# Kernel optimization log

Measured on AMD Instinct MI355X. Metric: run time of the kernel, lower is better.

## Reference

```python
import jax, jax.numpy as jnp
import numpy as np

MAX_TAG = 16          # tag ids live in [0, MAX_TAG]; 0 = background
NUM_SEG = MAX_TAG + 1
LGG_VALUE = 3.0


def setup_inputs() -> dict:
    key = jax.random.key(0)
    k1, k2, k3 = jax.random.split(key, 3)
    B, C, H, W = 16, 8, 512, 512
    gt_kernel_key = jax.random.randint(k1, (B, H, W), 0, MAX_TAG + 1, dtype=jnp.int32)
    training_mask = jax.random.randint(k2, (B, H, W), 0, 2, dtype=jnp.int32)
    similarity_vector = jax.random.normal(k3, (B, C, H, W), dtype=jnp.float32)
    return {
        "gt_kernel_key": gt_kernel_key,
        "training_mask": training_mask,
        "similarity_vector": similarity_vector,
    }


def _per_sample_loss(sim_hwc, gk, mask):
    # sim_hwc: [H, W, C]; gk, mask: [H, W]
    C = sim_hwc.shape[-1]
    flat_sim = sim_hwc.reshape(-1, C)            # [HW, C]
    flat_gk = gk.reshape(-1)                     # [HW]
    ones = jnp.ones_like(flat_gk, dtype=jnp.float32)

    # segment mean per tag over the UNMASKED kernel map (matches original:
    # tags are selected with the mask, but means use gt_kernel directly)
    sums = jax.ops.segment_sum(flat_sim, flat_gk, num_segments=NUM_SEG)      # [T, C]
    counts = jax.ops.segment_sum(ones, flat_gk, num_segments=NUM_SEG)       # [T]
    means = sums / jnp.maximum(counts, 1.0)[:, None]

    # a tag participates iff it appears in gt_kernel_key * training_mask and != 0
    masked_gk = flat_gk * mask.reshape(-1)
    masked_counts = jax.ops.segment_sum(ones, masked_gk, num_segments=NUM_SEG)
    present = (masked_counts > 0).at[0].set(False)                           # [T]

    # pairwise distances between tag means (tiny: NUM_SEG x NUM_SEG)
    diff = means[:, None, :] - means[None, :, :]                             # [T, T, C]
    dist = jnp.sqrt(jnp.sum(diff * diff, axis=-1) + 1e-12)                   # [T, T]
    pair_loss = jnp.log(jnp.maximum(LGG_VALUE - dist, 0.0) ** 2 + 1.0)

    valid = present[:, None] & present[None, :] & ~jnp.eye(NUM_SEG, dtype=bool)
    n_valid = jnp.sum(valid.astype(jnp.float32))
    loss = jnp.sum(jnp.where(valid, pair_loss, 0.0)) / jnp.maximum(n_valid, 1.0)
    sample_valid = (jnp.sum(present.astype(jnp.int32)) >= 2).astype(jnp.float32)
    return loss, sample_valid


def reference(gt_kernel_key, training_mask, similarity_vector):
    # [B, C, H, W] -> [B, H, W, C]
    sim = jnp.transpose(similarity_vector, (0, 2, 3, 1))
    losses, valids = jax.vmap(_per_sample_loss)(sim, gt_kernel_key, training_mask)
    n = jnp.sum(valids)
    return jnp.where(n > 0, jnp.sum(losses * valids) / jnp.maximum(n, 1.0), 0.0)
```

## Files before the change

### kernel.cpp

```cpp
#include <hip/hip_runtime.h>

#define NB 16
#define NC 8
#define HW (512*512)
#define NT 16
#define LGG 3.0f

#define BLOCKS 2048
#define THREADS 256
#define BPSAMP (BLOCKS/NB)
#define PXB (HW/BPSAMP)
#define PXW (PXB/4)
#define NMFMA (PXW/32)
#define NCOL 10
#define ACCW (NT*NCOL)

typedef __attribute__((ext_vector_type(8))) short bf16x8;
typedef __attribute__((ext_vector_type(4))) float f32x4;

__device__ __forceinline__ unsigned pk_bf16(float x, float y) {
    unsigned r;
    asm("v_cvt_pk_bf16_f32 %0, %1, %2" : "=v"(r) : "v"(x), "v"(y));
    return r;
}

struct Frag { int4 g0, g1, m0, m1; float4 v0, v1; };

__device__ __forceinline__ Frag ldm(const int* gkp, const int* mkp,
                                    const float* sp, int off, int c) {
    Frag f;
    f.g0 = *(const int4*)(gkp + off);
    f.g1 = *(const int4*)(gkp + off + 4);
    if (c < 8) {
        f.v0 = *(const float4*)(sp + off);
        f.v1 = *(const float4*)(sp + off + 4);
    }
    if (c == 9) {
        f.m0 = *(const int4*)(mkp + off);
        f.m1 = *(const int4*)(mkp + off + 4);
    }
    return f;
}

__device__ __forceinline__ unsigned onehot2(int a, int b, int r1) {
    return (a == r1 ? 0x3F80u : 0u) | (b == r1 ? 0x3F800000u : 0u);
}
__device__ __forceinline__ unsigned mask2(int a, int b) {
    return (a ? 0x3F80u : 0u) | (b ? 0x3F800000u : 0u);
}

__device__ __forceinline__ f32x4 step(const Frag& f, int c, int r1, f32x4 acc) {
    union { bf16x8 v; unsigned u[4]; } A, B;
    A.u[0] = onehot2(f.g0.x, f.g0.y, r1);
    A.u[1] = onehot2(f.g0.z, f.g0.w, r1);
    A.u[2] = onehot2(f.g1.x, f.g1.y, r1);
    A.u[3] = onehot2(f.g1.z, f.g1.w, r1);
    const unsigned bs0 = pk_bf16(f.v0.x, f.v0.y), bs1 = pk_bf16(f.v0.z, f.v0.w);
    const unsigned bs2 = pk_bf16(f.v1.x, f.v1.y), bs3 = pk_bf16(f.v1.z, f.v1.w);
    const unsigned bm0 = mask2(f.m0.x, f.m0.y), bm1 = mask2(f.m0.z, f.m0.w);
    const unsigned bm2 = mask2(f.m1.x, f.m1.y), bm3 = mask2(f.m1.z, f.m1.w);
    B.u[0] = c < 8 ? bs0 : (c == 8 ? 0x3F803F80u : (c == 9 ? bm0 : 0u));
    B.u[1] = c < 8 ? bs1 : (c == 8 ? 0x3F803F80u : (c == 9 ? bm1 : 0u));
    B.u[2] = c < 8 ? bs2 : (c == 8 ? 0x3F803F80u : (c == 9 ? bm2 : 0u));
    B.u[3] = c < 8 ? bs3 : (c == 8 ? 0x3F803F80u : (c == 9 ? bm3 : 0u));
    return __builtin_amdgcn_mfma_f32_16x16x32_bf16(A.v, B.v, acc, 0, 0, 0);
}

__global__ __launch_bounds__(256) void init_ws(float* g_acc) {
    const int i = threadIdx.x;
    #pragma unroll
    for (int k = 0; k < NB*ACCW; k += 256)
        if (k + i < NB*ACCW) g_acc[k + i] = 0.f;
}

__global__ __launch_bounds__(THREADS) void accum(
    const int* __restrict__ gk, const int* __restrict__ mask,
    const float* __restrict__ sim, float* __restrict__ g_acc)
{
    const int tid  = threadIdx.x;
    const int lane = tid & 63, wid = tid >> 6;
    const int bid  = blockIdx.x;
    const int b    = bid / BPSAMP;
    const int sb   = bid % BPSAMP;
    const int c    = lane & 15;
    const int l4   = lane >> 4;
    const int p0   = sb * PXB + wid * PXW + l4 * 8;

    const int*   gkp = gk   + (size_t)b * HW + p0;
    const int*   mkp = mask + (size_t)b * HW + p0;
    const float* sp  = sim  + ((size_t)b * NC + (c & 7)) * HW + p0;

    __shared__ float lred[4][256];

    f32x4 acc = {0.f, 0.f, 0.f, 0.f};
    const int r1 = c + 1;

    Frag cur = ldm(gkp, mkp, sp, 0, c);
    #pragma unroll
    for (int it = 0; it < NMFMA; ++it) {
        Frag nxt;
        if (it + 1 < NMFMA) nxt = ldm(gkp, mkp, sp, (it + 1) * 32, c);
        acc = step(cur, c, r1, acc);
        cur = nxt;
    }

    const int row0 = (lane >> 4) * 4;
    #pragma unroll
    for (int i = 0; i < 4; ++i) lred[wid][(row0 + i) * 16 + c] = acc[i];
    __syncthreads();

    if (tid < NT * NCOL) {
        const int r = tid / NCOL, cc = tid % NCOL;
        const float s = lred[0][r*16+cc] + lred[1][r*16+cc]
                      + lred[2][r*16+cc] + lred[3][r*16+cc];
        atomicAdd(&g_acc[b * ACCW + tid], s);
    }
}

__global__ __launch_bounds__(256) void finalize(
    const float* __restrict__ g_acc, float* __restrict__ out)
{
    __shared__ float    means[NB][NT][NC];
    __shared__ unsigned pres[NB];
    __shared__ float    sl[NB], sn[NB];
    const int tid = threadIdx.x;

    if (tid < NB) pres[tid] = 0u;
    __syncthreads();

    {
        const int b = tid >> 4, t = tid & 15;
        const float* row = g_acc + b * ACCW + t * NCOL;
        const float cnt = row[8];
        const float mc  = row[9];
        const float inv = 1.f / fmaxf(cnt, 1.f);
        #pragma unroll
        for (int cc = 0; cc < NC; ++cc) means[b][t][cc] = row[cc] * inv;
        if (mc > 0.5f) atomicOr(&pres[b], 1u << (t + 1));
    }
    __syncthreads();

    const int b = tid >> 4, i = tid & 15;
    const unsigned pr = pres[b];
    float loss = 0.f, nv = 0.f;
    if ((pr >> (i + 1)) & 1u) {
        #pragma unroll
        for (int j = 0; j < NT; ++j) {
            if (j != i && ((pr >> (j + 1)) & 1u)) {
                float d2 = 0.f;
                #pragma unroll
                for (int cc = 0; cc < NC; ++cc) {
                    const float d = means[b][i][cc] - means[b][j][cc];
                    d2 += d * d;
                }
                const float dist = sqrtf(d2 + 1e-12f);
                const float r = fmaxf(LGG - dist, 0.f);
                loss += logf(r * r + 1.f);
                nv += 1.f;
            }
        }
    }
    #pragma unroll
    for (int o = 8; o; o >>= 1) { loss += __shfl_xor(loss, o); nv += __shfl_xor(nv, o); }
    if (i == 0) {
        const float v = (__popc(pr) >= 2) ? 1.f : 0.f;
        sl[b] = v * (loss / fmaxf(nv, 1.f));
        sn[b] = v;
    }
    __syncthreads();
    if (tid == 0) {
        float tl = 0.f, tv = 0.f;
        for (int bb = 0; bb < NB; ++bb) { tl += sl[bb]; tv += sn[bb]; }
        out[0] = (tv > 0.f) ? tl / tv : 0.f;
    }
}

extern "C" void kernel_launch(void* const* d_in, const int* in_sizes, int n_in,
                              void* d_out, int out_size, void* d_ws, size_t ws_size,
                              hipStream_t stream) {
    const int*   gk   = (const int*)d_in[0];
    const int*   mask = (const int*)d_in[1];
    const float* sim  = (const float*)d_in[2];
    float* out   = (float*)d_out;
    float* g_acc = (float*)d_ws;

    init_ws<<<1, 256, 0, stream>>>(g_acc);
    accum<<<BLOCKS, THREADS, 0, stream>>>(gk, mask, sim, g_acc);
    finalize<<<1, 256, 0, stream>>>(g_acc, out);
}
```

Baseline: 54.54 us.

## Stage tag and similarity tiles into LDS via direct global-to-LDS loads

Replaces per-lane redundant global loads, where 16 lanes per pixel group each reloaded the same tag ids, with cooperative global_load_lds copies of tag and similarity planes into shared memory per 512-pixel tile. Waves then read fragments from LDS and feed the MFMA one-hot reduction, with only the mask still loaded from global. The aim is to cut duplicated global memory traffic, at the cost of two barriers per tile and no double buffering, so load latency is exposed between tiles.

```diff
diff --git a/kernel.cpp b/kernel.cpp
--- a/kernel.cpp
+++ b/kernel.cpp
@@ -10,10 +10,16 @@
 #define THREADS 256
 #define BPSAMP (BLOCKS/NB)
 #define PXB (HW/BPSAMP)
-#define PXW (PXB/4)
-#define NMFMA (PXW/32)
+#define TILE 512
+#define NTILES (PXB/TILE)
+#define JITERS (TILE/128)
+#define NCHUNK (2 + 2*NC)
 #define NCOL 10
 #define ACCW (NT*NCOL)
+
+#define SIM_LDS 2048
+#define PLANE_STRIDE 2064
+#define LDS_BYTES (SIM_LDS + NC*PLANE_STRIDE)
 
 typedef __attribute__((ext_vector_type(8))) short bf16x8;
 typedef __attribute__((ext_vector_type(4))) float f32x4;
@@ -24,24 +30,6 @@
     return r;
 }
 
-struct Frag { int4 g0, g1, m0, m1; float4 v0, v1; };
-
-__device__ __forceinline__ Frag ldm(const int* gkp, const int* mkp,
-                                    const float* sp, int off, int c) {
-    Frag f;
-    f.g0 = *(const int4*)(gkp + off);
-    f.g1 = *(const int4*)(gkp + off + 4);
-    if (c < 8) {
-        f.v0 = *(const float4*)(sp + off);
-        f.v1 = *(const float4*)(sp + off + 4);
-    }
-    if (c == 9) {
-        f.m0 = *(const int4*)(mkp + off);
-        f.m1 = *(const int4*)(mkp + off + 4);
-    }
-    return f;
-}
-
 __device__ __forceinline__ unsigned onehot2(int a, int b, int r1) {
     return (a == r1 ? 0x3F80u : 0u) | (b == r1 ? 0x3F800000u : 0u);
 }
@@ -49,21 +37,10 @@
     return (a ? 0x3F80u : 0u) | (b ? 0x3F800000u : 0u);
 }
 
-__device__ __forceinline__ f32x4 step(const Frag& f, int c, int r1, f32x4 acc) {
-    union { bf16x8 v; unsigned u[4]; } A, B;
-    A.u[0] = onehot2(f.g0.x, f.g0.y, r1);
-    A.u[1] = onehot2(f.g0.z, f.g0.w, r1);
-    A.u[2] = onehot2(f.g1.x, f.g1.y, r1);
-    A.u[3] = onehot2(f.g1.z, f.g1.w, r1);
-    const unsigned bs0 = pk_bf16(f.v0.x, f.v0.y), bs1 = pk_bf16(f.v0.z, f.v0.w);
-    const unsigned bs2 = pk_bf16(f.v1.x, f.v1.y), bs3 = pk_bf16(f.v1.z, f.v1.w);
-    const unsigned bm0 = mask2(f.m0.x, f.m0.y), bm1 = mask2(f.m0.z, f.m0.w);
-    const unsigned bm2 = mask2(f.m1.x, f.m1.y), bm3 = mask2(f.m1.z, f.m1.w);
-    B.u[0] = c < 8 ? bs0 : (c == 8 ? 0x3F803F80u : (c == 9 ? bm0 : 0u));
-    B.u[1] = c < 8 ? bs1 : (c == 8 ? 0x3F803F80u : (c == 9 ? bm1 : 0u));
-    B.u[2] = c < 8 ? bs2 : (c == 8 ? 0x3F803F80u : (c == 9 ? bm2 : 0u));
-    B.u[3] = c < 8 ? bs3 : (c == 8 ? 0x3F803F80u : (c == 9 ? bm3 : 0u));
-    return __builtin_amdgcn_mfma_f32_16x16x32_bf16(A.v, B.v, acc, 0, 0, 0);
+__device__ __forceinline__ void gload_lds16(const void* g, void* lds) {
+    __builtin_amdgcn_global_load_lds(
+        (const __attribute__((address_space(1))) void*)g,
+        (__attribute__((address_space(3))) void*)lds, 16, 0, 0);
 }
 
 __global__ __launch_bounds__(256) void init_ws(float* g_acc) {
@@ -84,35 +61,87 @@
     const int sb   = bid % BPSAMP;
     const int c    = lane & 15;
     const int l4   = lane >> 4;
-    const int p0   = sb * PXB + wid * PXW + l4 * 8;
-
-    const int*   gkp = gk   + (size_t)b * HW + p0;
-    const int*   mkp = mask + (size_t)b * HW + p0;
-    const float* sp  = sim  + ((size_t)b * NC + (c & 7)) * HW + p0;
-
-    __shared__ float lred[4][256];
+    const int base = sb * PXB;
+
+    __shared__ __align__(16) char ldsbuf[LDS_BYTES];
+
+    const int*   gkS = gk   + (size_t)b * HW + base;
+    const int*   mkS = mask + (size_t)b * HW + base;
+    const float* smS = sim  + (size_t)b * NC * HW + base;
 
     f32x4 acc = {0.f, 0.f, 0.f, 0.f};
     const int r1 = c + 1;
-
-    Frag cur = ldm(gkp, mkp, sp, 0, c);
+    const int simoff = SIM_LDS + (c & 7) * PLANE_STRIDE;
+
+    for (int t = 0; t < NTILES; ++t) {
+        const int t0 = t * TILE;
+        #pragma unroll
+        for (int k = 0; k < 5; ++k) {
+            const int idx = wid + 4 * k;
+            if (idx < NCHUNK) {
+                const void* src;
+                int dst;
+                if (idx < 2) {
+                    src = gkS + t0 + idx * 256 + lane * 4;
+                    dst = idx * 1024;
+                } else {
+                    const int p = (idx - 2) >> 1, h = (idx - 2) & 1;
+                    src = smS + (size_t)p * HW + t0 + h * 256 + lane * 4;
+                    dst = SIM_LDS + p * PLANE_STRIDE + h * 1024;
+                }
+                gload_lds16(src, ldsbuf + dst);
+            }
+        }
+        int4 mc0, mc1;
+        if (c == 9) {
+            const int* mp = mkS + t0 + wid * 128 + l4 * 8;
+            mc0 = *(const int4*)mp; mc1 = *(const int4*)(mp + 4);
+        }
+        __syncthreads();
+
+        #pragma unroll
+        for (int j = 0; j < JITERS; ++j) {
+            int4 mn0, mn1;
+            if (j + 1 < JITERS && c == 9) {
+                const int* mp = mkS + t0 + wid * 128 + (j + 1) * 32 + l4 * 8;
+                mn0 = *(const int4*)mp; mn1 = *(const int4*)(mp + 4);
+            }
+            const int px = wid * 128 + j * 32 + l4 * 8;
+            const int4 g0 = *(const int4*)(ldsbuf + px * 4);
+            const int4 g1 = *(const int4*)(ldsbuf + px * 4 + 16);
+            const float4 v0 = *(const float4*)(ldsbuf + simoff + px * 4);
+            const float4 v1 = *(const float4*)(ldsbuf + simoff + px * 4 + 16);
+
+            union { bf16x8 v; unsigned u[4]; } A, B;
+            A.u[0] = onehot2(g0.x, g0.y, r1);
+            A.u[1] = onehot2(g0.z, g0.w, r1);
+            A.u[2] = onehot2(g1.x, g1.y, r1);
+            A.u[3] = onehot2(g1.z, g1.w, r1);
+            const unsigned bs0 = pk_bf16(v0.x, v0.y), bs1 = pk_bf16(v0.z, v0.w);
+            const unsigned bs2 = pk_bf16(v1.x, v1.y), bs3 = pk_bf16(v1.z, v1.w);
+            const unsigned bm0 = mask2(mc0.x, mc0.y), bm1 = mask2(mc0.z, mc0.w);
+            const unsigned bm2 = mask2(mc1.x, mc1.y), bm3 = mask2(mc1.z, mc1.w);
+            B.u[0] = c < 8 ? bs0 : (c == 8 ? 0x3F803F80u : (c == 9 ? bm0 : 0u));
+            B.u[1] = c < 8 ? bs1 : (c == 8 ? 0x3F803F80u : (c == 9 ? bm1 : 0u));
+            B.u[2] = c < 8 ? bs2 : (c == 8 ? 0x3F803F80u : (c == 9 ? bm2 : 0u));
+            B.u[3] = c < 8 ? bs3 : (c == 8 ? 0x3F803F80u : (c == 9 ? bm3 : 0u));
+
+            acc = __builtin_amdgcn_mfma_f32_16x16x32_bf16(A.v, B.v, acc, 0, 0, 0);
+            mc0 = mn0; mc1 = mn1;
+        }
+        __syncthreads();
+    }
+
+    float* lred = (float*)ldsbuf;
+    const int row0 = l4 * 4;
     #pragma unroll
-    for (int it = 0; it < NMFMA; ++it) {
-        Frag nxt;
-        if (it + 1 < NMFMA) nxt = ldm(gkp, mkp, sp, (it + 1) * 32, c);
-        acc = step(cur, c, r1, acc);
-        cur = nxt;
-    }
-
-    const int row0 = (lane >> 4) * 4;
-    #pragma unroll
-    for (int i = 0; i < 4; ++i) lred[wid][(row0 + i) * 16 + c] = acc[i];
+    for (int i = 0; i < 4; ++i) lred[wid * 256 + (row0 + i) * 16 + c] = acc[i];
     __syncthreads();
 
     if (tid < NT * NCOL) {
         const int r = tid / NCOL, cc = tid % NCOL;
-        const float s = lred[0][r*16+cc] + lred[1][r*16+cc]
-                      + lred[2][r*16+cc] + lred[3][r*16+cc];
+        const float s = lred[0*256 + r*16 + cc] + lred[1*256 + r*16 + cc]
+                      + lred[2*256 + r*16 + cc] + lred[3*256 + r*16 + cc];
         atomicAdd(&g_acc[b * ACCW + tid], s);
     }
 }
```

Result: faster. 44.99 us (-17.5%).
